# Optimization experiments

Hardware: AMD Instinct MI355X
Metric: run time of the kernel (lower is better)

## Reference

```python
import jax, jax.numpy as jnp
import numpy as np

N_NODES = 50000
N_EDGES = 800000
EMB = 128
N_LAYERS = 2
BN_EPS = 1e-5


def setup_inputs() -> dict:
    key = jax.random.key(0)
    ks = jax.random.split(key, 16)
    N, E, D, L = N_NODES, N_EDGES, EMB, N_LAYERS
    x = jax.random.randint(ks[0], (N, 2), 0, 3)
    edge_index = jax.random.randint(ks[1], (2, E), 0, N)
    edge_attr = jax.random.randint(ks[2], (E, 2), 0, 3)
    batch = jnp.zeros((N,), dtype=jnp.int32)
    s = 0.1
    xemb1 = jax.random.normal(ks[3], (120, D)) * s   # atom-type embedding
    xemb2 = jax.random.normal(ks[4], (3, D)) * s     # chirality embedding
    e1 = jax.random.normal(ks[5], (L, 7, D)) * s     # bond-type embedding per layer
    e2 = jax.random.normal(ks[6], (L, 3, D)) * s     # bond-direction embedding per layer
    W1 = jax.random.normal(ks[7], (L, D, 2 * D)) * s
    b1 = jnp.zeros((L, 2 * D))
    W2 = jax.random.normal(ks[8], (L, 2 * D, D)) * s
    b2 = jnp.zeros((L, D))
    gamma = jnp.ones((L, D))
    beta = jnp.zeros((L, D))
    return {"x": x, "edge_index": edge_index, "edge_attr": edge_attr, "batch": batch,
            "xemb1": xemb1, "xemb2": xemb2, "e1": e1, "e2": e2,
            "W1": W1, "b1": b1, "W2": W2, "b2": b2, "gamma": gamma, "beta": beta}


def _gnn_forward(x, edge_index, edge_attr, xemb1, xemb2, e1, e2, W1, b1, W2, b2, gamma, beta):
    N = x.shape[0]
    # add self loops; self-loop edge_attr = [4, 0]
    loop = jnp.arange(N, dtype=edge_index.dtype)
    src = jnp.concatenate([edge_index[0], loop])
    dst = jnp.concatenate([edge_index[1], loop])
    loop_attr = jnp.concatenate([jnp.full((N, 1), 4, dtype=edge_attr.dtype),
                                 jnp.zeros((N, 1), dtype=edge_attr.dtype)], axis=1)
    ea = jnp.concatenate([edge_attr, loop_attr], axis=0)  # [E+N, 2]

    # input node embedding
    h = xemb1[x[:, 0]] + xemb2[x[:, 1]]  # [N, D]

    for l in range(N_LAYERS):
        eemb = e1[l][ea[:, 0]] + e2[l][ea[:, 1]]      # [E+N, D]
        msg = h[src] + eemb                            # gather + edge fuse
        agg = jax.ops.segment_sum(msg, dst, num_segments=N)  # scatter-add
        # GIN update MLP: Linear -> ReLU -> Linear
        h2 = jax.nn.relu(agg @ W1[l] + b1[l]) @ W2[l] + b2[l]
        # BatchNorm1d (training mode: biased batch stats)
        mu = jnp.mean(h2, axis=0)
        var = jnp.mean(jnp.square(h2 - mu), axis=0)
        h2 = gamma[l] * (h2 - mu) * jax.lax.rsqrt(var + BN_EPS) + beta[l]
        # dropout(relu) for non-final layers; drop_ratio=0 -> identity dropout
        h = h2 if l == N_LAYERS - 1 else jax.nn.relu(h2)
    return h  # JK='last'


def reference(x, edge_index, edge_attr, batch, xemb1, xemb2, e1, e2, W1, b1, W2, b2, gamma, beta):
    return _gnn_forward(x, edge_index, edge_attr, xemb1, xemb2, e1, e2, W1, b1, W2, b2, gamma, beta)
```

## Files before the change

kernel.cpp:

```cpp
#include <hip/hip_runtime.h>
#include <stdint.h>

#define N_NODES 50000
#define N_EDGES 800000
#define EMB 128
#define NPAD 50176
#define MBLK 392
#define BN_EPS 1e-5f
#define SENT_KEY ((N_NODES << 5) | 21)
#define NODES_PER_XCD 6250
#define XCHUNK 2048
#define NCHUNKS ((N_EDGES + XCHUNK - 1) / XCHUNK)
#define PBLK 196

typedef __attribute__((ext_vector_type(8))) short short8;
typedef __attribute__((ext_vector_type(4))) float f32x4;

__device__ __forceinline__ unsigned short f2bf(float f) {
    unsigned int u = __float_as_uint(f);
    u += 0x7fffu + ((u >> 16) & 1u);
    return (unsigned short)(u >> 16);
}
__device__ __forceinline__ float bflo(unsigned int v) { return __uint_as_float(v << 16); }
__device__ __forceinline__ float bfhi(unsigned int v) { return __uint_as_float(v & 0xffff0000u); }
__device__ __forceinline__ unsigned int packbf(float lo, float hi) {
    return (unsigned int)f2bf(lo) | ((unsigned int)f2bf(hi) << 16);
}

__global__ void k_prep(const int* __restrict__ x, const float* __restrict__ xe1,
                       const float* __restrict__ xe2, unsigned int* __restrict__ h,
                       const float* __restrict__ W1, const float* __restrict__ W2,
                       unsigned short* __restrict__ w1t, unsigned short* __restrict__ w2t,
                       int* __restrict__ deg,
                       const int* __restrict__ ei, const int* __restrict__ ea,
                       int* __restrict__ keyv, float* __restrict__ bnsum,
                       int* __restrict__ bmeta) {
    int idx = blockIdx.x * 256 + threadIdx.x;
    int i = idx >> 6, j = idx & 63;
    if (i < N_NODES) {
        int a = x[2 * i], c = x[2 * i + 1];
        float2 va = *(const float2*)(xe1 + a * EMB + j * 2);
        float2 vb = *(const float2*)(xe2 + c * EMB + j * 2);
        h[i * 64 + j] = packbf(va.x + vb.x, va.y + vb.y);
    } else if (i == N_NODES) {
        h[(size_t)i * 64 + j] = 0u;
    }
    if (idx < 4 * 32768) {
        int sec = idx >> 15, q = idx & 32767;
        if (sec < 2) {
            int r = q >> 8, c = q & 255;
            w1t[sec * 32768 + c * 128 + r] = f2bf(W1[sec * 32768 + q]);
        } else {
            int s = sec - 2;
            int r = q >> 7, c = q & 127;
            w2t[s * 32768 + c * 256 + r] = f2bf(W2[s * 32768 + q]);
        }
    }
    if (idx < N_EDGES) {
        int2 aa = *(const int2*)(ea + 2 * idx);
        keyv[idx] = (ei[idx] << 5) | (aa.x * 3 + aa.y);
    }
    if (idx < N_NODES) deg[idx] = 0;
    if (idx < 512) bnsum[idx] = 0.f;
    if (idx < 16) bmeta[idx] = 0;
}

__global__ void k_hist(const int* __restrict__ dst, int* __restrict__ deg) {
    int xcd = blockIdx.x & 7, chunk = blockIdx.x >> 3;
    int lo = xcd * NODES_PER_XCD, hi = lo + NODES_PER_XCD;
    int e0 = chunk * XCHUNK + threadIdx.x * 4;
#pragma unroll
    for (int it = 0; it < XCHUNK / 1024; ++it) {
        int e = e0 + it * 1024;
        if (e < N_EDGES) {
            int4 d4 = *(const int4*)(dst + e);
            if (d4.x >= lo && d4.x < hi) atomicAdd(&deg[d4.x], 1);
            if (d4.y >= lo && d4.y < hi) atomicAdd(&deg[d4.y], 1);
            if (d4.z >= lo && d4.z < hi) atomicAdd(&deg[d4.z], 1);
            if (d4.w >= lo && d4.w < hi) atomicAdd(&deg[d4.w], 1);
        }
    }
}

__global__ void k_scan1(const int* __restrict__ deg, int* __restrict__ part, int* __restrict__ bsums) {
    __shared__ int wsum[16];
    int lane = threadIdx.x & 63, wid = threadIdx.x >> 6;
    int i = blockIdx.x * 1024 + threadIdx.x;
    int d = (i < N_NODES) ? deg[i] : 0;
    int v = (d + 15) & ~15;
    int s = v;
#pragma unroll
    for (int off = 1; off < 64; off <<= 1) {
        int t = __shfl_up(s, off);
        if (lane >= off) s += t;
    }
    if (lane == 63) wsum[wid] = s;
    __syncthreads();
    if (wid == 0) {
        int w = (lane < 16) ? wsum[lane] : 0;
#pragma unroll
        for (int off = 1; off < 16; off <<= 1) {
            int t = __shfl_up(w, off);
            if (lane >= off) w += t;
        }
        if (lane < 16) wsum[lane] = w;
    }
    __syncthreads();
    int base = (wid > 0) ? wsum[wid - 1] : 0;
    if (i < N_NODES) part[i] = base + s - v;
    if (threadIdx.x == 1023) bsums[blockIdx.x] = wsum[15];
}

__global__ void k_scan3(const int* __restrict__ part, const int* __restrict__ bsums,
                        const int* __restrict__ deg, int* __restrict__ offs,
                        int* __restrict__ cursor, int* __restrict__ keys,
                        int* __restrict__ bcnt) {
    __shared__ int bs[64];
    __shared__ int lc[8];
    int tid = threadIdx.x;
    if (tid < 8) lc[tid] = 0;
    if (tid < 64) {
        int v = (tid < 49) ? bsums[tid] : 0;
        int orig = v;
#pragma unroll
        for (int off = 1; off < 64; off <<= 1) {
            int t = __shfl_up(v, off);
            if (tid >= off) v += t;
        }
        bs[tid] = v - orig;
    }
    __syncthreads();
    int i = blockIdx.x * 256 + tid;
    if (i < N_NODES) {
        int o = part[i] + bs[i >> 10];
        offs[i] = o;
        cursor[i] = o;
        int d = deg[i], pd = (d + 15) & ~15;
        for (int j = d; j < pd; ++j) keys[o + j] = SENT_KEY;
        if (i == N_NODES - 1) offs[N_NODES] = o + pd;
        int nch = pd >> 4;
        atomicAdd(&lc[nch > 7 ? 7 : nch], 1);
    }
    __syncthreads();
    if (tid < 8) atomicAdd(&bcnt[tid], lc[tid]);
}

__global__ void k_fill(const int* __restrict__ dst, const int* __restrict__ keyv,
                       int* __restrict__ cursor, int* __restrict__ keys,
                       const int* __restrict__ deg, const int* __restrict__ bcnt,
                       int* __restrict__ bcur, int* __restrict__ perm) {
    int xcd = blockIdx.x & 7, chunk = blockIdx.x >> 3;
    int lo = xcd * NODES_PER_XCD, hi = lo + NODES_PER_XCD;
    int e0 = chunk * XCHUNK + threadIdx.x * 4;
#pragma unroll
    for (int it = 0; it < XCHUNK / 1024; ++it) {
        int e = e0 + it * 1024;
        if (e < N_EDGES) {
            int4 d4 = *(const int4*)(dst + e);
            int dv[4] = {d4.x, d4.y, d4.z, d4.w};
#pragma unroll
            for (int q = 0; q < 4; ++q) {
                int d = dv[q];
                if (d >= lo && d < hi) {
                    int p = atomicAdd(&cursor[d], 1);
                    keys[p] = keyv[e + q];
                }
            }
        }
    }
    if (blockIdx.x < PBLK) {
        __shared__ int lcnt[8], gbase[8], tbase[8];
        if (threadIdx.x < 8) lcnt[threadIdx.x] = 0;
        __syncthreads();
        int i = blockIdx.x * 256 + threadIdx.x;
        int b = 0, lrank = 0;
        if (i < N_NODES) {
            int nch = (deg[i] + 15) >> 4;
            b = nch > 7 ? 7 : nch;
            lrank = atomicAdd(&lcnt[b], 1);
        }
        __syncthreads();
        if (threadIdx.x < 8) {
            gbase[threadIdx.x] = atomicAdd(&bcur[threadIdx.x], lcnt[threadIdx.x]);
            int s = 0;
            for (int k = 0; k < threadIdx.x; ++k) s += bcnt[k];
            tbase[threadIdx.x] = s;
        }
        __syncthreads();
        if (i < N_NODES) perm[tbase[b] + gbase[b] + lrank] = i;
    }
}

__global__ __launch_bounds__(256, 4) void k_agg(
    const unsigned int* __restrict__ h,
    const int* __restrict__ offs,
    const int* __restrict__ keys,
    const int* __restrict__ perm,
    const float* __restrict__ e1l, const float* __restrict__ e2l,
    unsigned int* __restrict__ agg)
{
    __shared__ float e12[22 * 132];
    for (int t = threadIdx.x; t < 22 * 128; t += 256) {
        int combo = t >> 7, f = t & 127;
        float v = 0.f;
        if (combo < 21) {
            int a0 = combo / 3, a1 = combo - a0 * 3;
            v = e1l[a0 * EMB + f] + e2l[a1 * EMB + f];
        }
        e12[combo * 132 + f] = v;
    }
    __syncthreads();
    int wave = threadIdx.x >> 6, lane = threadIdx.x & 63;
    int sub = lane >> 4, fl = lane & 15;
    int wi = blockIdx.x * 4 + wave;
    int q = (wi & 255) * 49 + (wi >> 8);
    int slot = q * 4 + sub;
    int node = (slot < N_NODES) ? perm[slot] : slot;
    float ax[8] = {0.f, 0.f, 0.f, 0.f, 0.f, 0.f, 0.f, 0.f};
    int o = 0, nch = 0;
    if (node < N_NODES) {
        o = offs[node];
        nch = (offs[node + 1] - o) >> 4;
        uint4 hv = *(const uint4*)(h + (size_t)node * 64 + fl * 4);
        const float* ep = e12 + 12 * 132 + fl * 8;
        float4 e0 = *(const float4*)ep, e1_ = *(const float4*)(ep + 4);
        ax[0] = bflo(hv.x) + e0.x;  ax[1] = bfhi(hv.x) + e0.y;
        ax[2] = bflo(hv.y) + e0.z;  ax[3] = bfhi(hv.y) + e0.w;
        ax[4] = bflo(hv.z) + e1_.x; ax[5] = bfhi(hv.z) + e1_.y;
        ax[6] = bflo(hv.w) + e1_.z; ax[7] = bfhi(hv.w) + e1_.w;
    }
    int maxch = nch;
#pragma unroll
    for (int d = 32; d; d >>= 1) maxch = max(maxch, __shfl_xor(maxch, d));
    int key = (0 < nch) ? keys[o + fl] : SENT_KEY;
    for (int c = 0; c < maxch; ++c) {
        int keyn = (c + 1 < nch) ? keys[o + (c + 1) * 16 + fl] : SENT_KEY;
        int kjA[8], kjB[8];
        uint4 g[8];
#pragma unroll
        for (int j = 0; j < 8; ++j) {
            kjA[j] = __shfl(key, sub * 16 + j);
            g[j] = *(const uint4*)(h + (size_t)(kjA[j] >> 5) * 64 + fl * 4);
        }
#pragma unroll
        for (int j = 0; j < 8; ++j) {
            uint4 gg = g[j];
            kjB[j] = __shfl(key, sub * 16 + 8 + j);
            g[j] = *(const uint4*)(h + (size_t)(kjB[j] >> 5) * 64 + fl * 4);
            const float* ep = e12 + (kjA[j] & 31) * 132 + fl * 8;
            float4 e0 = *(const float4*)ep, e1_ = *(const float4*)(ep + 4);
            ax[0] += bflo(gg.x) + e0.x;  ax[1] += bfhi(gg.x) + e0.y;
            ax[2] += bflo(gg.y) + e0.z;  ax[3] += bfhi(gg.y) + e0.w;
            ax[4] += bflo(gg.z) + e1_.x; ax[5] += bfhi(gg.z) + e1_.y;
            ax[6] += bflo(gg.w) + e1_.z; ax[7] += bfhi(gg.w) + e1_.w;
        }
#pragma unroll
        for (int j = 0; j < 8; ++j) {
            uint4 gg = g[j];
            const float* ep = e12 + (kjB[j] & 31) * 132 + fl * 8;
            float4 e0 = *(const float4*)ep, e1_ = *(const float4*)(ep + 4);
            ax[0] += bflo(gg.x) + e0.x;  ax[1] += bfhi(gg.x) + e0.y;
            ax[2] += bflo(gg.y) + e0.z;  ax[3] += bfhi(gg.y) + e0.w;
            ax[4] += bflo(gg.z) + e1_.x; ax[5] += bfhi(gg.z) + e1_.y;
            ax[6] += bflo(gg.w) + e1_.z; ax[7] += bfhi(gg.w) + e1_.w;
        }
        key = keyn;
    }
    {
        uint4 out;
        out.x = packbf(ax[0], ax[1]); out.y = packbf(ax[2], ax[3]);
        out.z = packbf(ax[4], ax[5]); out.w = packbf(ax[6], ax[7]);
        *(uint4*)(agg + (size_t)node * 64 + fl * 4) = out;
    }
}

__global__ __launch_bounds__(256, 2) void k_mlp(
    unsigned short* aggh2,
    const unsigned short* __restrict__ w1t,
    const float* __restrict__ b1,
    const unsigned short* __restrict__ w2t,
    const float* __restrict__ b2,
    float* __restrict__ bnsum)
{
    __shared__ float bn[256];
    int lane = threadIdx.x & 63;
    int wave = threadIdx.x >> 6;
    int quad = lane >> 4, r16 = lane & 15;
    int m0 = (blockIdx.x * 4 + wave) * 32;
    int sel  = (lane >> 5) & 1;
    int srcA = ((lane >> 4) & 1) * 32 + r16;
    int srcB = srcA + 16;
    bn[threadIdx.x] = 0.f;

    short8 bagg[2][4];
#pragma unroll
    for (int t = 0; t < 2; ++t)
#pragma unroll
        for (int c = 0; c < 4; ++c)
            bagg[t][c] = *(const short8*)(aggh2 + (size_t)(m0 + t * 16 + r16) * 128 + c * 32 + quad * 8);

    float b2v[8];
#pragma unroll
    for (int n = 0; n < 8; ++n) b2v[n] = b2[n * 16 + r16];

    f32x4 acc2[2][8];
#pragma unroll
    for (int t = 0; t < 2; ++t)
#pragma unroll
        for (int n = 0; n < 8; ++n) acc2[t][n] = (f32x4){0.f, 0.f, 0.f, 0.f};

    for (int c2 = 0; c2 < 8; ++c2) {
        unsigned int pk[2][2][2];
#pragma unroll
        for (int ntl = 0; ntl < 2; ++ntl) {
            int nt = c2 * 2 + ntl;
            short8 aw[4];
#pragma unroll
            for (int c = 0; c < 4; ++c)
                aw[c] = *(const short8*)(w1t + (nt * 16 + r16) * 128 + c * 32 + quad * 8);
            float4 bv = *(const float4*)(b1 + nt * 16 + quad * 4);
#pragma unroll
            for (int t = 0; t < 2; ++t) {
                f32x4 a1 = {0.f, 0.f, 0.f, 0.f};
#pragma unroll
                for (int c = 0; c < 4; ++c)
                    a1 = __builtin_amdgcn_mfma_f32_16x16x32_bf16(aw[c], bagg[t][c], a1, 0, 0, 0);
                float v0 = a1[0] + bv.x; v0 = v0 > 0.f ? v0 : 0.f;
                float v1 = a1[1] + bv.y; v1 = v1 > 0.f ? v1 : 0.f;
                float v2 = a1[2] + bv.z; v2 = v2 > 0.f ? v2 : 0.f;
                float v3 = a1[3] + bv.w; v3 = v3 > 0.f ? v3 : 0.f;
                pk[ntl][t][0] = packbf(v0, v1);
                pk[ntl][t][1] = packbf(v2, v3);
            }
        }
        short8 a2f[2];
#pragma unroll
        for (int t = 0; t < 2; ++t) {
            int u0 = __shfl((int)pk[0][t][0], srcA), w0 = __shfl((int)pk[1][t][0], srcA);
            int u1 = __shfl((int)pk[0][t][1], srcA), w1_ = __shfl((int)pk[1][t][1], srcA);
            int u2 = __shfl((int)pk[0][t][0], srcB), w2_ = __shfl((int)pk[1][t][0], srcB);
            int u3 = __shfl((int)pk[0][t][1], srcB), w3_ = __shfl((int)pk[1][t][1], srcB);
            union { int i[4]; short8 s; } a2u;
            a2u.i[0] = sel ? w0 : u0;
            a2u.i[1] = sel ? w1_ : u1;
            a2u.i[2] = sel ? w2_ : u2;
            a2u.i[3] = sel ? w3_ : u3;
            a2f[t] = a2u.s;
        }
#pragma unroll
        for (int n = 0; n < 8; ++n) {
            short8 bw = *(const short8*)(w2t + (n * 16 + r16) * 256 + c2 * 32 + quad * 8);
            acc2[0][n] = __builtin_amdgcn_mfma_f32_16x16x32_bf16(a2f[0], bw, acc2[0][n], 0, 0, 0);
            acc2[1][n] = __builtin_amdgcn_mfma_f32_16x16x32_bf16(a2f[1], bw, acc2[1][n], 0, 0, 0);
        }
    }
    float s[8], q[8];
#pragma unroll
    for (int n = 0; n < 8; ++n) { s[n] = 0.f; q[n] = 0.f; }
#pragma unroll
    for (int t = 0; t < 2; ++t)
#pragma unroll
        for (int n = 0; n < 8; ++n)
#pragma unroll
            for (int r = 0; r < 4; ++r) {
                int row = m0 + t * 16 + quad * 4 + r;
                float v = acc2[t][n][r] + b2v[n];
                if (row < N_NODES) {
                    aggh2[(size_t)row * 128 + n * 16 + r16] = f2bf(v);
                    s[n] += v; q[n] += v * v;
                }
            }
#pragma unroll
    for (int n = 0; n < 8; ++n) {
        s[n] += __shfl_xor(s[n], 16); q[n] += __shfl_xor(q[n], 16);
        s[n] += __shfl_xor(s[n], 32); q[n] += __shfl_xor(q[n], 32);
    }
    __syncthreads();
    if (quad == 0) {
#pragma unroll
        for (int n = 0; n < 8; ++n) {
            atomicAdd(&bn[n * 16 + r16], s[n]);
            atomicAdd(&bn[128 + n * 16 + r16], q[n]);
        }
    }
    __syncthreads();
    atomicAdd(&bnsum[threadIdx.x], bn[threadIdx.x]);
}

__global__ void k_bnnorm(const uint4* __restrict__ h2, const float* __restrict__ bnsum,
                         const float* __restrict__ gamma, const float* __restrict__ beta,
                         uint4* __restrict__ outb, float4* __restrict__ outf, int mode) {
    __shared__ float ab[256];
    int tid = threadIdx.x;
    if (tid < 128) {
        float mean = bnsum[tid] * (1.f / N_NODES);
        float var  = bnsum[128 + tid] * (1.f / N_NODES) - mean * mean;
        float rstd = rsqrtf(var + BN_EPS);
        float g = gamma[tid];
        ab[tid]       = g * rstd;
        ab[128 + tid] = beta[tid] - mean * g * rstd;
    }
    __syncthreads();
    int idx = blockIdx.x * 256 + tid;
    if (idx >= N_NODES * 16) return;
    int p = (idx & 15) * 8;
    uint4 hv = h2[idx];
    float v0 = bflo(hv.x) * ab[p + 0] + ab[128 + p + 0];
    float v1 = bfhi(hv.x) * ab[p + 1] + ab[128 + p + 1];
    float v2 = bflo(hv.y) * ab[p + 2] + ab[128 + p + 2];
    float v3 = bfhi(hv.y) * ab[p + 3] + ab[128 + p + 3];
    float v4 = bflo(hv.z) * ab[p + 4] + ab[128 + p + 4];
    float v5 = bfhi(hv.z) * ab[p + 5] + ab[128 + p + 5];
    float v6 = bflo(hv.w) * ab[p + 6] + ab[128 + p + 6];
    float v7 = bfhi(hv.w) * ab[p + 7] + ab[128 + p + 7];
    if (mode == 0) {
        v0 = v0 > 0.f ? v0 : 0.f; v1 = v1 > 0.f ? v1 : 0.f;
        v2 = v2 > 0.f ? v2 : 0.f; v3 = v3 > 0.f ? v3 : 0.f;
        v4 = v4 > 0.f ? v4 : 0.f; v5 = v5 > 0.f ? v5 : 0.f;
        v6 = v6 > 0.f ? v6 : 0.f; v7 = v7 > 0.f ? v7 : 0.f;
        uint4 out;
        out.x = packbf(v0, v1); out.y = packbf(v2, v3);
        out.z = packbf(v4, v5); out.w = packbf(v6, v7);
        outb[idx] = out;
    } else {
        outf[2 * idx]     = make_float4(v0, v1, v2, v3);
        outf[2 * idx + 1] = make_float4(v4, v5, v6, v7);
    }
}

extern "C" void kernel_launch(void* const* d_in, const int* in_sizes, int n_in,
                              void* d_out, int out_size, void* d_ws, size_t ws_size,
                              hipStream_t stream) {
    const int* x  = (const int*)d_in[0];
    const int* ei = (const int*)d_in[1];
    const int* ea = (const int*)d_in[2];
    const float* xe1 = (const float*)d_in[4];
    const float* xe2 = (const float*)d_in[5];
    const float* e1  = (const float*)d_in[6];
    const float* e2  = (const float*)d_in[7];
    const float* W1  = (const float*)d_in[8];
    const float* b1  = (const float*)d_in[9];
    const float* W2  = (const float*)d_in[10];
    const float* b2  = (const float*)d_in[11];
    const float* gm  = (const float*)d_in[12];
    const float* bt  = (const float*)d_in[13];

    char* ws = (char*)d_ws;
    size_t off = 0;
    auto take = [&](size_t bytes) -> char* {
        char* p = ws + off;
        off = (off + bytes + 255) & ~(size_t)255;
        return p;
    };
    unsigned int* h_buf = (unsigned int*)take((size_t)(N_NODES + 1) * 64 * 4);
    unsigned int* aggb  = (unsigned int*)take((size_t)NPAD * 64 * 4);
    unsigned short* w1t = (unsigned short*)take((size_t)2 * 32768 * 2);
    unsigned short* w2t = (unsigned short*)take((size_t)2 * 32768 * 2);
    int* deg    = (int*)take((size_t)N_NODES * 4);
    int* offs   = (int*)take((size_t)(N_NODES + 1) * 4);
    int* cursor = (int*)take((size_t)N_NODES * 4);
    int* keys   = (int*)take((size_t)(N_EDGES + N_NODES * 16) * 4);
    int* keyv   = (int*)take((size_t)N_EDGES * 4);
    int* bsums  = (int*)take(64 * 4);
    float* bnsum = (float*)take(512 * 4);
    int* bmeta  = (int*)take(16 * 4);
    int* perm   = (int*)take((size_t)N_NODES * 4);
    int* bcnt = bmeta, *bcur = bmeta + 8;

    k_prep<<<((N_NODES + 1) * 64 + 255) / 256, 256, 0, stream>>>(x, xe1, xe2, h_buf,
                                                                 W1, W2, w1t, w2t, deg,
                                                                 ei, ea, keyv, bnsum, bmeta);
    k_hist<<<8 * NCHUNKS, 256, 0, stream>>>(ei + N_EDGES, deg);
    k_scan1<<<49, 1024, 0, stream>>>(deg, offs, bsums);
    k_scan3<<<(N_NODES + 255) / 256, 256, 0, stream>>>(offs, bsums, deg, offs, cursor, keys, bcnt);
    k_fill<<<8 * NCHUNKS, 256, 0, stream>>>(ei + N_EDGES, keyv, cursor, keys,
                                            deg, bcnt, bcur, perm);

    for (int l = 0; l < 2; ++l) {
        k_agg<<<NPAD / 16, 256, 0, stream>>>(h_buf, offs, keys, perm,
                                             e1 + l * 896, e2 + l * 384, aggb);
        k_mlp<<<MBLK, 256, 0, stream>>>((unsigned short*)aggb, w1t + l * 32768, b1 + l * 256,
                                        w2t + l * 32768, b2 + l * 128, bnsum + l * 256);
        k_bnnorm<<<(N_NODES * 16 + 255) / 256, 256, 0, stream>>>((const uint4*)aggb, bnsum + l * 256,
                                                                 gm + l * 128, bt + l * 128,
                                                                 (uint4*)h_buf, (float4*)d_out, l);
    }
}
```

Before: 373.7 us.

## Fuse degree histogram into prep and replace two-pass scan with atomic block allocation

The degree histogram moves into the prep kernel as a plain atomic per edge, and the zeroing of deg, BN sums and metadata moves to a single memset. The two-kernel prefix scan becomes one k_alloc kernel that claims each block's CSR region with an atomic on a global cursor, so node segments are no longer in node order. k_agg now derives the chunk count from deg rather than the offset difference. This cuts the launch count and removes a dependent scan pass, but the histogram atomics are no longer partitioned by XCD and the CSR layout loses its ordering, which could hurt locality.

```diff
diff --git a/kernel.cpp b/kernel.cpp
--- a/kernel.cpp
+++ b/kernel.cpp
@@ -33,8 +33,7 @@
                        unsigned short* __restrict__ w1t, unsigned short* __restrict__ w2t,
                        int* __restrict__ deg,
                        const int* __restrict__ ei, const int* __restrict__ ea,
-                       int* __restrict__ keyv, float* __restrict__ bnsum,
-                       int* __restrict__ bmeta) {
+                       int* __restrict__ keyv) {
     int idx = blockIdx.x * 256 + threadIdx.x;
     int i = idx >> 6, j = idx & 63;
     if (i < N_NODES) {
@@ -59,85 +58,39 @@
     if (idx < N_EDGES) {
         int2 aa = *(const int2*)(ea + 2 * idx);
         keyv[idx] = (ei[idx] << 5) | (aa.x * 3 + aa.y);
-    }
-    if (idx < N_NODES) deg[idx] = 0;
-    if (idx < 512) bnsum[idx] = 0.f;
-    if (idx < 16) bmeta[idx] = 0;
-}
-
-__global__ void k_hist(const int* __restrict__ dst, int* __restrict__ deg) {
-    int xcd = blockIdx.x & 7, chunk = blockIdx.x >> 3;
-    int lo = xcd * NODES_PER_XCD, hi = lo + NODES_PER_XCD;
-    int e0 = chunk * XCHUNK + threadIdx.x * 4;
-#pragma unroll
-    for (int it = 0; it < XCHUNK / 1024; ++it) {
-        int e = e0 + it * 1024;
-        if (e < N_EDGES) {
-            int4 d4 = *(const int4*)(dst + e);
-            if (d4.x >= lo && d4.x < hi) atomicAdd(&deg[d4.x], 1);
-            if (d4.y >= lo && d4.y < hi) atomicAdd(&deg[d4.y], 1);
-            if (d4.z >= lo && d4.z < hi) atomicAdd(&deg[d4.z], 1);
-            if (d4.w >= lo && d4.w < hi) atomicAdd(&deg[d4.w], 1);
-        }
-    }
-}
-
-__global__ void k_scan1(const int* __restrict__ deg, int* __restrict__ part, int* __restrict__ bsums) {
-    __shared__ int wsum[16];
-    int lane = threadIdx.x & 63, wid = threadIdx.x >> 6;
-    int i = blockIdx.x * 1024 + threadIdx.x;
+        atomicAdd(&deg[ei[N_EDGES + idx]], 1);
+    }
+}
+
+__global__ void k_alloc(const int* __restrict__ deg, int* __restrict__ gcur,
+                        int* __restrict__ offs, int* __restrict__ cursor,
+                        int* __restrict__ keys, int* __restrict__ bcnt) {
+    __shared__ int wbase[4];
+    __shared__ int lc[8];
+    int tid = threadIdx.x, lane = tid & 63, wid = tid >> 6;
+    if (tid < 8) lc[tid] = 0;
+    int i = blockIdx.x * 256 + tid;
     int d = (i < N_NODES) ? deg[i] : 0;
-    int v = (d + 15) & ~15;
-    int s = v;
+    int pd = (d + 15) & ~15;
+    int s = pd;
 #pragma unroll
     for (int off = 1; off < 64; off <<= 1) {
         int t = __shfl_up(s, off);
         if (lane >= off) s += t;
     }
-    if (lane == 63) wsum[wid] = s;
-    __syncthreads();
-    if (wid == 0) {
-        int w = (lane < 16) ? wsum[lane] : 0;
-#pragma unroll
-        for (int off = 1; off < 16; off <<= 1) {
-            int t = __shfl_up(w, off);
-            if (lane >= off) w += t;
-        }
-        if (lane < 16) wsum[lane] = w;
-    }
-    __syncthreads();
-    int base = (wid > 0) ? wsum[wid - 1] : 0;
-    if (i < N_NODES) part[i] = base + s - v;
-    if (threadIdx.x == 1023) bsums[blockIdx.x] = wsum[15];
-}
-
-__global__ void k_scan3(const int* __restrict__ part, const int* __restrict__ bsums,
-                        const int* __restrict__ deg, int* __restrict__ offs,
-                        int* __restrict__ cursor, int* __restrict__ keys,
-                        int* __restrict__ bcnt) {
-    __shared__ int bs[64];
-    __shared__ int lc[8];
-    int tid = threadIdx.x;
-    if (tid < 8) lc[tid] = 0;
-    if (tid < 64) {
-        int v = (tid < 49) ? bsums[tid] : 0;
-        int orig = v;
-#pragma unroll
-        for (int off = 1; off < 64; off <<= 1) {
-            int t = __shfl_up(v, off);
-            if (tid >= off) v += t;
-        }
-        bs[tid] = v - orig;
-    }
-    __syncthreads();
-    int i = blockIdx.x * 256 + tid;
+    if (lane == 63) wbase[wid] = s;
+    __syncthreads();
+    if (tid == 0) {
+        int t0 = wbase[0], t1 = wbase[1], t2 = wbase[2], t3 = wbase[3];
+        int b = atomicAdd(gcur, t0 + t1 + t2 + t3);
+        wbase[0] = b; wbase[1] = b + t0; wbase[2] = b + t0 + t1; wbase[3] = b + t0 + t1 + t2;
+    }
+    __syncthreads();
     if (i < N_NODES) {
-        int o = part[i] + bs[i >> 10];
+        int o = wbase[wid] + s - pd;
         offs[i] = o;
         cursor[i] = o;
-        int d = deg[i], pd = (d + 15) & ~15;
         for (int j = d; j < pd; ++j) keys[o + j] = SENT_KEY;
-        if (i == N_NODES - 1) offs[N_NODES] = o + pd;
         int nch = pd >> 4;
         atomicAdd(&lc[nch > 7 ? 7 : nch], 1);
     }
@@ -194,6 +147,7 @@
 __global__ __launch_bounds__(256, 4) void k_agg(
     const unsigned int* __restrict__ h,
     const int* __restrict__ offs,
+    const int* __restrict__ deg,
     const int* __restrict__ keys,
     const int* __restrict__ perm,
     const float* __restrict__ e1l, const float* __restrict__ e2l,
@@ -220,7 +174,7 @@
     int o = 0, nch = 0;
     if (node < N_NODES) {
         o = offs[node];
-        nch = (offs[node + 1] - o) >> 4;
+        nch = (deg[node] + 15) >> 4;
         uint4 hv = *(const uint4*)(h + (size_t)node * 64 + fl * 4);
         const float* ep = e12 + 12 * 132 + fl * 8;
         float4 e0 = *(const float4*)ep, e1_ = *(const float4*)(ep + 4);
@@ -456,28 +410,27 @@
     unsigned int* aggb  = (unsigned int*)take((size_t)NPAD * 64 * 4);
     unsigned short* w1t = (unsigned short*)take((size_t)2 * 32768 * 2);
     unsigned short* w2t = (unsigned short*)take((size_t)2 * 32768 * 2);
-    int* deg    = (int*)take((size_t)N_NODES * 4);
+    int* zbuf   = (int*)take((size_t)(N_NODES + 512 + 32) * 4);
+    int* deg    = zbuf;
+    float* bnsum = (float*)(zbuf + N_NODES);
+    int* bmeta  = zbuf + N_NODES + 512;
     int* offs   = (int*)take((size_t)(N_NODES + 1) * 4);
     int* cursor = (int*)take((size_t)N_NODES * 4);
     int* keys   = (int*)take((size_t)(N_EDGES + N_NODES * 16) * 4);
     int* keyv   = (int*)take((size_t)N_EDGES * 4);
-    int* bsums  = (int*)take(64 * 4);
-    float* bnsum = (float*)take(512 * 4);
-    int* bmeta  = (int*)take(16 * 4);
     int* perm   = (int*)take((size_t)N_NODES * 4);
-    int* bcnt = bmeta, *bcur = bmeta + 8;
-
+    int* bcnt = bmeta, *bcur = bmeta + 8, *gcur = bmeta + 16;
+
+    hipMemsetAsync(zbuf, 0, (size_t)(N_NODES + 512 + 32) * 4, stream);
     k_prep<<<((N_NODES + 1) * 64 + 255) / 256, 256, 0, stream>>>(x, xe1, xe2, h_buf,
                                                                  W1, W2, w1t, w2t, deg,
-                                                                 ei, ea, keyv, bnsum, bmeta);
-    k_hist<<<8 * NCHUNKS, 256, 0, stream>>>(ei + N_EDGES, deg);
-    k_scan1<<<49, 1024, 0, stream>>>(deg, offs, bsums);
-    k_scan3<<<(N_NODES + 255) / 256, 256, 0, stream>>>(offs, bsums, deg, offs, cursor, keys, bcnt);
+                                                                 ei, ea, keyv);
+    k_alloc<<<PBLK, 256, 0, stream>>>(deg, gcur, offs, cursor, keys, bcnt);
     k_fill<<<8 * NCHUNKS, 256, 0, stream>>>(ei + N_EDGES, keyv, cursor, keys,
                                             deg, bcnt, bcur, perm);
 
     for (int l = 0; l < 2; ++l) {
-        k_agg<<<NPAD / 16, 256, 0, stream>>>(h_buf, offs, keys, perm,
+        k_agg<<<NPAD / 16, 256, 0, stream>>>(h_buf, offs, deg, keys, perm,
                                              e1 + l * 896, e2 + l * 384, aggb);
         k_mlp<<<MBLK, 256, 0, stream>>>((unsigned short*)aggb, w1t + l * 32768, b1 + l * 256,
                                         w2t + l * 32768, b2 + l * 128, bnsum + l * 256);
```

Result: faster. 365.6 us (-2.2%).
